# Kernel optimization log

Hardware: AMD Instinct MI355X
Metric: run time of the kernel (lower is better)

The kernel has to match this reference:

```python
import jax, jax.numpy as jnp
import numpy as np

DIM = 384
HEADS = 12
WS = 7
HID = 4 * 256  # FFN hidden is hard-coded default 1024, NOT 4*dim
EPS = 1e-5


def layernorm(x, g, b):
    mu = jnp.mean(x, axis=-1, keepdims=True)
    var = jnp.mean(jnp.square(x - mu), axis=-1, keepdims=True)
    return (x - mu) * jax.lax.rsqrt(var + EPS) * g + b


def setup_inputs() -> dict:
    key = jax.random.key(0)
    ks = jax.random.split(key, 12)
    s = 0.02
    return {
        "x": jax.random.normal(ks[0], (32, DIM, 56, 56), dtype=jnp.float32),
        "ln1_g": jnp.ones((DIM,), jnp.float32),
        "ln1_b": jnp.zeros((DIM,), jnp.float32),
        "qkv_w": jax.random.normal(ks[1], (3 * DIM, DIM), jnp.float32) * s,
        "qkv_b": jnp.zeros((3 * DIM,), jnp.float32),
        "proj_w": jax.random.normal(ks[2], (DIM, DIM), jnp.float32) * s,
        "proj_b": jnp.zeros((DIM,), jnp.float32),
        "ln2_g": jnp.ones((DIM,), jnp.float32),
        "ln2_b": jnp.zeros((DIM,), jnp.float32),
        "fc1_w": jax.random.normal(ks[3], (HID, DIM), jnp.float32) * s,
        "fc1_b": jnp.zeros((HID,), jnp.float32),
        "fc2_w": jax.random.normal(ks[4], (DIM, HID), jnp.float32) * s,
        "fc2_b": jnp.zeros((DIM,), jnp.float32),
    }


def window_attention(x, qkv_w, qkv_b, proj_w, proj_b):
    # x: [B, H, W, C] channels-last
    B, H, W, C = x.shape
    Wh, Ww = H // WS, W // WS
    # partition: [B*Wh*Ww, WS*WS, C]
    w = x.reshape(B, Wh, WS, Ww, WS, C).transpose(0, 1, 3, 2, 4, 5)
    w = w.reshape(B * Wh * Ww, WS * WS, C)
    Bn, N, _ = w.shape
    hd = C // HEADS
    qkv = w @ qkv_w.T + qkv_b  # [Bn, N, 3C]
    qkv = qkv.reshape(Bn, N, 3, HEADS, hd).transpose(2, 0, 3, 1, 4)
    q, k, v = qkv[0], qkv[1], qkv[2]  # each [Bn, h, N, hd]
    attn = jnp.einsum('bhnd,bhmd->bhnm', q, k) * (hd ** -0.5)
    attn = jax.nn.softmax(attn, axis=-1)
    o = jnp.einsum('bhnm,bhmd->bhnd', attn, v)
    o = o.transpose(0, 2, 1, 3).reshape(Bn, N, C)
    o = o @ proj_w.T + proj_b
    # reverse
    o = o.reshape(B, Wh, Ww, WS, WS, C).transpose(0, 1, 3, 2, 4, 5)
    return o.reshape(B, H, W, C)


def reference(x, ln1_g, ln1_b, qkv_w, qkv_b, proj_w, proj_b,
              ln2_g, ln2_b, fc1_w, fc1_b, fc2_w, fc2_b):
    # x: [B, C, H, W]
    residual = x
    h = x.transpose(0, 2, 3, 1)  # [B,H,W,C]
    h = layernorm(h, ln1_g, ln1_b)
    h = window_attention(h, qkv_w, qkv_b, proj_w, proj_b)
    x = h.transpose(0, 3, 1, 2) + residual
    residual = x
    h = x.transpose(0, 2, 3, 1)
    h = layernorm(h, ln2_g, ln2_b)
    h = jax.nn.gelu(h @ fc1_w.T + fc1_b, approximate=False)
    h = h @ fc2_w.T + fc2_b
    return h.transpose(0, 3, 1, 2) + residual
```

## Files before the change

kernel.cpp:

```cpp
#include <hip/hip_runtime.h>
#include <cstdint>
#include <cmath>

#define DIM 384
#define HEADS 12
#define TOKENS 100352
#define HW_ 3136
#define NWIN 2048

typedef __attribute__((ext_vector_type(8))) short short8;
typedef __attribute__((ext_vector_type(4))) short short4v;
typedef __attribute__((ext_vector_type(2))) short short2v;
typedef __attribute__((ext_vector_type(4))) float f32x4;

#define AS1 __attribute__((address_space(1)))
#define AS3 __attribute__((address_space(3)))

__device__ __forceinline__ short f2b(float f){
  unsigned u = __builtin_bit_cast(unsigned, f);
  u += 0x7FFFu + ((u >> 16) & 1u);
  return (short)(u >> 16);
}
__device__ __forceinline__ float b2f(short h){
  unsigned u = ((unsigned)(unsigned short)h) << 16;
  return __builtin_bit_cast(float, u);
}

__device__ __forceinline__ void gload_lds16(const short* g, short* l){
  __builtin_amdgcn_global_load_lds((AS1 void*)(g), (AS3 void*)(l), 16, 0, 0);
}

__global__ void k_cvt(const float* __restrict__ s, short* __restrict__ d, int n){
  int i = blockIdx.x*256 + threadIdx.x;
  if (i < n) d[i] = f2b(s[i]);
}

__global__ __launch_bounds__(256) void k_ln1(const float* __restrict__ x,
    const float* __restrict__ gam, const float* __restrict__ bet,
    short* __restrict__ ln1, short* __restrict__ xr)
{
  __shared__ float red0[256];
  __shared__ float red1[256];
  __shared__ float mus[64], rss[64];
  __shared__ short lnc[64*36];
  __shared__ short xc[64*36];
  int t = threadIdx.x;
  int blk = blockIdx.x;
  int b = blk / 49;
  int hw0 = (blk % 49) * 64;
  int p = t & 63, cq = t >> 6;
  const float* xb = x + (long)b*DIM*HW_ + hw0 + p;
  float s = 0.f, sq = 0.f;
  for (int i = 0; i < 96; i++){
    int c = i*4 + cq;
    float v = xb[(long)c*HW_];
    s += v; sq += v*v;
  }
  red0[t] = s; red1[t] = sq;
  __syncthreads();
  if (t < 64){
    float ts = red0[t] + red0[t+64] + red0[t+128] + red0[t+192];
    float tq = red1[t] + red1[t+64] + red1[t+128] + red1[t+192];
    float mu = ts * (1.f/DIM);
    float var = tq * (1.f/DIM) - mu*mu;
    mus[t] = mu;
    rss[t] = rsqrtf(var + 1e-5f);
  }
  __syncthreads();
  float mu_p = mus[p], rs_p = rss[p];
  int p2 = t >> 2, q4 = t & 3;
  int hwp2 = hw0 + p2;
  int h2 = hwp2 / 56, w2 = hwp2 % 56;
  int wt2 = ((b*8 + h2/7)*8 + w2/7)*49 + (h2%7)*7 + (w2%7);
  long lnbase = (long)wt2*DIM;
  long xrbase = (long)(b*HW_ + hwp2)*DIM;
  for (int cc0 = 0; cc0 < DIM; cc0 += 32){
    #pragma unroll
    for (int u = 0; u < 8; u++){
      int c = cc0 + cq*8 + u;
      float v = xb[(long)c*HW_];
      float nv = (v - mu_p)*rs_p*gam[c] + bet[c];
      lnc[p*36 + cq*8 + u] = f2b(nv);
      xc[p*36 + cq*8 + u] = f2b(v);
    }
    __syncthreads();
    short8 av, bv;
    #pragma unroll
    for (int u = 0; u < 8; u++){
      av[u] = lnc[p2*36 + q4*8 + u];
      bv[u] = xc[p2*36 + q4*8 + u];
    }
    *(short8*)(ln1 + lnbase + cc0 + q4*8) = av;
    *(short8*)(xr + xrbase + cc0 + q4*8) = bv;
    __syncthreads();
  }
}

#define EPI_BIAS 0
#define EPI_PROJ 1
#define EPI_GELU 2
#define EPI_RES  3

template<int EPI>
__global__ __launch_bounds__(256) void k_gemm(
    const short* __restrict__ A, const short* __restrict__ B,
    const float* __restrict__ bias, short* __restrict__ out,
    const short* __restrict__ res, int M, int N, int K, int ntiles)
{
  __shared__ float smemf[8448];
  short* AsP = (short*)smemf;
  short* BsP = (short*)(smemf + 4096);
  float* E   = smemf;

  int nwg = gridDim.x;
  int orig = blockIdx.x;
  int bid = (orig & 7) * (nwg >> 3) + (orig >> 3);
  int nt = bid % ntiles, mt = bid / ntiles;
  int m0 = mt*128, n0 = nt*128;
  int t = threadIdx.x;
  int lane = t & 63, wv = t >> 6;
  int wm = wv >> 1, wn = wv & 1;
  int gg = lane >> 4, cc = lane & 15;

  int srow = t >> 2;
  int skc = ((t & 3) ^ (srow & 3)) << 3;
  const short* Ab = A + (long)(m0 + srow)*K + skc;
  const short* Bb = B + (long)(n0 + srow)*K + skc;
  long rowstep = 64L*K;

  int goff = (gg << 3) ^ ((cc & 3) << 3);

  f32x4 acc[4][4];
  #pragma unroll
  for (int i=0;i<4;i++)
    #pragma unroll
    for (int j=0;j<4;j++) acc[i][j] = (f32x4){0.f,0.f,0.f,0.f};

  gload_lds16(Ab,           AsP + t*8);
  gload_lds16(Ab + rowstep, AsP + (t+256)*8);
  gload_lds16(Bb,           BsP + t*8);
  gload_lds16(Bb + rowstep, BsP + (t+256)*8);

  int nk = K >> 5;
  for (int kt = 0; kt < nk; kt++){
    int cur = kt & 1;
    __syncthreads();
    if (kt + 1 < nk){
      int nxt = cur ^ 1;
      long ko = (long)(kt + 1) << 5;
      gload_lds16(Ab + ko,           AsP + nxt*4096 + t*8);
      gload_lds16(Ab + ko + rowstep, AsP + nxt*4096 + (t+256)*8);
      gload_lds16(Bb + ko,           BsP + nxt*4096 + t*8);
      gload_lds16(Bb + ko + rowstep, BsP + nxt*4096 + (t+256)*8);
    }
    const short* Ac = AsP + cur*4096;
    const short* Bc = BsP + cur*4096;
    short8 af[4], bfv[4];
    #pragma unroll
    for (int mi=0;mi<4;mi++) af[mi] = *(const short8*)(Ac + (wm*64 + mi*16 + cc)*32 + goff);
    #pragma unroll
    for (int ni=0;ni<4;ni++) bfv[ni] = *(const short8*)(Bc + (wn*64 + ni*16 + cc)*32 + goff);
    #pragma unroll
    for (int mi=0;mi<4;mi++)
      #pragma unroll
      for (int ni=0;ni<4;ni++)
        acc[mi][ni] = __builtin_amdgcn_mfma_f32_16x16x32_bf16(af[mi], bfv[ni], acc[mi][ni], 0, 0, 0);
  }

  #pragma unroll
  for (int p = 0; p < 2; p++){
    __syncthreads();
    #pragma unroll
    for (int mh = 0; mh < 2; mh++){
      #pragma unroll
      for (int r = 0; r < 4; r++){
        int crow = wm*32 + mh*16 + gg*4 + r;
        float* Er = E + crow*132 + wn*64 + cc;
        Er[0]  = acc[mh*2 + p][0][r];
        Er[16] = acc[mh*2 + p][1][r];
        Er[32] = acc[mh*2 + p][2][r];
        Er[48] = acc[mh*2 + p][3][r];
      }
    }
    __syncthreads();
    #pragma unroll
    for (int jj = 0; jj < 8; jj++){
      int unit = jj*256 + t;
      int crow = unit >> 5, chunk = unit & 31;
      int rr = crow & 15, mh = (crow >> 4) & 1, wmr = crow >> 5;
      int row = m0 + wmr*64 + (mh*2 + p)*16 + rr;
      int col = n0 + chunk*4;
      f32x4 v = *(const f32x4*)(E + crow*132 + chunk*4);
      f32x4 bv = *(const f32x4*)(bias + col);
      long orow;
      if constexpr (EPI == EPI_PROJ) {
        int b = row / HW_; int rem = row % HW_;
        int wid = rem / 49, idx = rem % 49;
        int hh = (wid >> 3)*7 + idx/7;
        int ww = (wid & 7)*7 + idx%7;
        orow = (long)(b*HW_ + hh*56 + ww)*N;
      } else {
        orow = (long)row*N;
      }
      float vv[4];
      #pragma unroll
      for (int j = 0; j < 4; j++){
        vv[j] = v[j] + bv[j];
        if constexpr (EPI == EPI_GELU)
          vv[j] = 0.5f*vv[j]*(1.f + erff(vv[j]*0.70710678118654752f));
      }
      if constexpr (EPI == EPI_PROJ || EPI == EPI_RES){
        short4v rv = *(const short4v*)(res + orow + col);
        #pragma unroll
        for (int j = 0; j < 4; j++) vv[j] += b2f(rv[j]);
      }
      short4v ov;
      #pragma unroll
      for (int j = 0; j < 4; j++) ov[j] = f2b(vv[j]);
      *(short4v*)(out + orow + col) = ov;
    }
  }
}

__global__ __launch_bounds__(256) void k_attn(const short* __restrict__ qkv, short* __restrict__ o)
{
  __shared__ short lds[4*7424];
  int t = threadIdx.x;
  int lane = t & 63, wv = t >> 6;
  int w = blockIdx.x;
  short* Qs = lds + wv*7424;
  short* Ks = Qs + 2560;
  short* Vt = Ks + 2560;
  short* Pl = Qs;
  int g = lane >> 4, c = lane & 15;
  int nrow = lane >> 2;
  int dc = (lane & 3) * 8;
  const float scale = 0.17677669529663687f;
  for (int hh = 0; hh < 3; hh++){
    int h = wv + hh*4;
    __syncthreads();
    long base = (long)w*49*1152 + h*32;
    #pragma unroll
    for (int it = 0; it < 4; it++){
      int n = it*16 + nrow;
      short8 vq = {0,0,0,0,0,0,0,0};
      short8 vk = vq, vvv = vq;
      if (n < 49){
        vq  = *(const short8*)(qkv + base + (long)n*1152 + dc);
        vk  = *(const short8*)(qkv + base + (long)n*1152 + 384 + dc);
        vvv = *(const short8*)(qkv + base + (long)n*1152 + 768 + dc);
      }
      *(short8*)(Qs + n*40 + dc) = vq;
      *(short8*)(Ks + n*40 + dc) = vk;
      #pragma unroll
      for (int u = 0; u < 8; u++) Vt[(dc+u)*72 + n] = vvv[u];
    }
    __syncthreads();
    f32x4 sacc[4][4];
    #pragma unroll
    for (int i=0;i<4;i++)
      #pragma unroll
      for (int j=0;j<4;j++) sacc[i][j] = (f32x4){0.f,0.f,0.f,0.f};
    short8 kf[4];
    #pragma unroll
    for (int ni=0;ni<4;ni++) kf[ni] = *(const short8*)(Ks + (ni*16 + c)*40 + g*8);
    #pragma unroll
    for (int mi=0;mi<4;mi++){
      short8 a = *(const short8*)(Qs + (mi*16 + c)*40 + g*8);
      #pragma unroll
      for (int ni=0;ni<4;ni++)
        sacc[mi][ni] = __builtin_amdgcn_mfma_f32_16x16x32_bf16(a, kf[ni], sacc[mi][ni], 0, 0, 0);
    }
    #pragma unroll
    for (int mi=0;mi<4;mi++){
      #pragma unroll
      for (int r=0;r<4;r++){
        float v0 = sacc[mi][0][r]*scale;
        float v1 = sacc[mi][1][r]*scale;
        float v2 = sacc[mi][2][r]*scale;
        float v3 = (c >= 1) ? -1e30f : sacc[mi][3][r]*scale;
        float mx = fmaxf(fmaxf(v0,v1), fmaxf(v2,v3));
        #pragma unroll
        for (int off=1; off<16; off<<=1) mx = fmaxf(mx, __shfl_xor(mx, off));
        float e0 = __expf(v0-mx), e1 = __expf(v1-mx), e2 = __expf(v2-mx), e3 = __expf(v3-mx);
        float sm = e0+e1+e2+e3;
        #pragma unroll
        for (int off=1; off<16; off<<=1) sm += __shfl_xor(sm, off);
        float inv = 1.f/sm;
        int prow = mi*16 + g*4 + r;
        Pl[prow*72 +      c] = f2b(e0*inv);
        Pl[prow*72 + 16 + c] = f2b(e1*inv);
        Pl[prow*72 + 32 + c] = f2b(e2*inv);
        Pl[prow*72 + 48 + c] = f2b(e3*inv);
      }
    }
    __syncthreads();
    f32x4 oacc[4][2];
    #pragma unroll
    for (int i=0;i<4;i++){ oacc[i][0] = (f32x4){0.f,0.f,0.f,0.f}; oacc[i][1] = oacc[i][0]; }
    #pragma unroll
    for (int ks=0; ks<2; ks++){
      short8 bb0 = *(const short8*)(Vt + (c)*72      + ks*32 + g*8);
      short8 bb1 = *(const short8*)(Vt + (16 + c)*72 + ks*32 + g*8);
      #pragma unroll
      for (int mi=0;mi<4;mi++){
        short8 aa = *(const short8*)(Pl + (mi*16 + c)*72 + ks*32 + g*8);
        oacc[mi][0] = __builtin_amdgcn_mfma_f32_16x16x32_bf16(aa, bb0, oacc[mi][0], 0, 0, 0);
        oacc[mi][1] = __builtin_amdgcn_mfma_f32_16x16x32_bf16(aa, bb1, oacc[mi][1], 0, 0, 0);
      }
    }
    #pragma unroll
    for (int mi=0;mi<4;mi++){
      #pragma unroll
      for (int r=0;r<4;r++){
        int row = mi*16 + g*4 + r;
        if (row < 49){
          long ob = ((long)w*49 + row)*384 + h*32;
          o[ob + c]      = f2b(oacc[mi][0][r]);
          o[ob + 16 + c] = f2b(oacc[mi][1][r]);
        }
      }
    }
  }
}

__global__ __launch_bounds__(256) void k_ln2(const short* __restrict__ x2,
  const float* __restrict__ gam, const float* __restrict__ bet, short* __restrict__ o)
{
  int t = threadIdx.x, lane = t & 63, wv = t >> 6;
  long row = (long)blockIdx.x*4 + wv;
  const short* xr = x2 + row*DIM;
  short4v a = *(const short4v*)(xr + lane*4);
  short2v b2 = *(const short2v*)(xr + 256 + lane*2);
  float f[6] = {b2f(a[0]),b2f(a[1]),b2f(a[2]),b2f(a[3]),b2f(b2[0]),b2f(b2[1])};
  float s = 0.f, sq = 0.f;
  #pragma unroll
  for (int i=0;i<6;i++){ s += f[i]; sq += f[i]*f[i]; }
  #pragma unroll
  for (int off=1; off<64; off<<=1){ s += __shfl_xor(s, off); sq += __shfl_xor(sq, off); }
  float mu = s*(1.f/DIM);
  float var = sq*(1.f/DIM) - mu*mu;
  float rs = rsqrtf(var + 1e-5f);
  int c0 = lane*4, c1 = 256 + lane*2;
  short4v oa; short2v ob;
  #pragma unroll
  for (int i=0;i<4;i++) oa[i] = f2b((f[i]-mu)*rs*gam[c0+i] + bet[c0+i]);
  #pragma unroll
  for (int j=0;j<2;j++) ob[j] = f2b((f[4+j]-mu)*rs*gam[c1+j] + bet[c1+j]);
  *(short4v*)(o + row*DIM + c0) = oa;
  *(short2v*)(o + row*DIM + c1) = ob;
}

__global__ __launch_bounds__(256) void k_out(const short* __restrict__ s, float* __restrict__ o)
{
  __shared__ short tile[64*392];
  int t = threadIdx.x;
  long tok0 = (long)blockIdx.x*64;
  int b = (int)(tok0 / HW_), hw0 = (int)(tok0 % HW_);
  #pragma unroll
  for (int i=0;i<12;i++){
    int unit = i*256 + t;
    int tok = unit / 48, slot = unit % 48;
    short8 v = *(const short8*)(s + (tok0+tok)*DIM + slot*8);
    int slotS = slot ^ (tok & 3);
    *(short8*)(tile + tok*392 + slotS*8) = v;
  }
  __syncthreads();
  int p = t & 63;
  int cq = t >> 6;
  for (int j=0;j<96;j++){
    int c = j*4 + cq;
    int sw = (c >> 3) ^ (p & 3);
    o[((long)b*DIM + c)*HW_ + hw0 + p] = b2f(tile[p*392 + sw*8 + (c & 7)]);
  }
}

extern "C" void kernel_launch(void* const* d_in, const int* in_sizes, int n_in,
                              void* d_out, int out_size, void* d_ws, size_t ws_size,
                              hipStream_t stream) {
  (void)in_sizes; (void)n_in; (void)out_size; (void)ws_size;
  const float* x      = (const float*)d_in[0];
  const float* ln1_g  = (const float*)d_in[1];
  const float* ln1_b  = (const float*)d_in[2];
  const float* qkv_w  = (const float*)d_in[3];
  const float* qkv_b  = (const float*)d_in[4];
  const float* proj_w = (const float*)d_in[5];
  const float* proj_b = (const float*)d_in[6];
  const float* ln2_g  = (const float*)d_in[7];
  const float* ln2_b  = (const float*)d_in[8];
  const float* fc1_w  = (const float*)d_in[9];
  const float* fc1_b  = (const float*)d_in[10];
  const float* fc2_w  = (const float*)d_in[11];
  const float* fc2_b  = (const float*)d_in[12];

  char* ws = (char*)d_ws;
  short* buf1 = (short*)(ws);
  short* buf2 = (short*)(ws + 231211008L);
  short* buf3 = (short*)(ws + 308281344L);
  short* buf4 = (short*)(ws + 385351680L);
  short* buf5 = (short*)(ws + 462422016L);
  short* wq = (short*)(ws + 539492352L);
  short* wp = wq + 442368;
  short* w1 = wp + 147456;
  short* w2 = w1 + 393216;

  k_cvt<<<dim3((442368+255)/256), dim3(256), 0, stream>>>(qkv_w, wq, 442368);
  k_cvt<<<dim3((147456+255)/256), dim3(256), 0, stream>>>(proj_w, wp, 147456);
  k_cvt<<<dim3((393216+255)/256), dim3(256), 0, stream>>>(fc1_w, w1, 393216);
  k_cvt<<<dim3((393216+255)/256), dim3(256), 0, stream>>>(fc2_w, w2, 393216);

  k_ln1<<<dim3(1568), dim3(256), 0, stream>>>(x, ln1_g, ln1_b, buf2, buf5);

  k_gemm<EPI_BIAS><<<dim3(784*9), dim3(256), 0, stream>>>(buf2, wq, qkv_b, buf1, nullptr,
                                                          TOKENS, 1152, 384, 9);
  k_attn<<<dim3(NWIN), dim3(256), 0, stream>>>(buf1, buf3);

  k_gemm<EPI_PROJ><<<dim3(784*3), dim3(256), 0, stream>>>(buf3, wp, proj_b, buf4, buf5,
                                                          TOKENS, 384, 384, 3);
  k_ln2<<<dim3(TOKENS/4), dim3(256), 0, stream>>>(buf4, ln2_g, ln2_b, buf2);

  k_gemm<EPI_GELU><<<dim3(784*8), dim3(256), 0, stream>>>(buf2, w1, fc1_b, buf1, nullptr,
                                                          TOKENS, 1024, 384, 8);
  k_gemm<EPI_RES><<<dim3(784*3), dim3(256), 0, stream>>>(buf1, w2, fc2_b, buf3, buf4,
                                                         TOKENS, 384, 1024, 3);
  k_out<<<dim3(1568), dim3(256), 0, stream>>>(buf3, (float*)d_out);
}
```

Before: 795.8 us.

## Enlarge GEMM tiles to 256x128 with three-stage LDS pipeline

Each GEMM workgroup now computes a 256x128 output tile instead of 128x128, which halves the grid sizes and raises reuse of the B operand. LDS is now split into three buffers, loads run two stages ahead, and explicit vmcnt waits replace the per-step syncthreads. The XOR swizzle on LDS tile addresses is removed, and launch bounds now ask for two waves per SIMD. The change trades higher register and LDS use, and possible LDS bank conflicts from the unswizzled layout, for fewer global loads and more overlap of memory latency.

```diff
diff --git a/kernel.cpp b/kernel.cpp
--- a/kernel.cpp
+++ b/kernel.cpp
@@ -101,85 +101,85 @@
 #define EPI_GELU 2
 #define EPI_RES  3
 
+__device__ __forceinline__ void stage_tile(const short* __restrict__ A,
+    const short* __restrict__ B, int K, int m0, int n0, int kk,
+    short* buf, int t)
+{
+  int rowA = t >> 2, slot = (t & 3) << 3;
+  const short* As = A + (long)(m0 + rowA)*K + kk + slot;
+  gload_lds16(As,                buf + t*8);
+  gload_lds16(As + 64L*K,        buf + (t+256)*8);
+  gload_lds16(As + 128L*K,       buf + (t+512)*8);
+  gload_lds16(As + 192L*K,       buf + (t+768)*8);
+  const short* Bs = B + (long)(n0 + rowA)*K + kk + slot;
+  gload_lds16(Bs,                buf + 8192 + t*8);
+  gload_lds16(Bs + 64L*K,        buf + 8192 + (t+256)*8);
+}
+
 template<int EPI>
-__global__ __launch_bounds__(256) void k_gemm(
+__global__ __launch_bounds__(256, 2) void k_gemm(
     const short* __restrict__ A, const short* __restrict__ B,
     const float* __restrict__ bias, short* __restrict__ out,
     const short* __restrict__ res, int M, int N, int K, int ntiles)
 {
-  __shared__ float smemf[8448];
-  short* AsP = (short*)smemf;
-  short* BsP = (short*)(smemf + 4096);
-  float* E   = smemf;
+  __shared__ short sbuf[36864];
+  float* E = (float*)sbuf;
 
   int nwg = gridDim.x;
   int orig = blockIdx.x;
   int bid = (orig & 7) * (nwg >> 3) + (orig >> 3);
   int nt = bid % ntiles, mt = bid / ntiles;
-  int m0 = mt*128, n0 = nt*128;
+  int m0 = mt*256, n0 = nt*128;
   int t = threadIdx.x;
   int lane = t & 63, wv = t >> 6;
   int wm = wv >> 1, wn = wv & 1;
   int gg = lane >> 4, cc = lane & 15;
 
-  int srow = t >> 2;
-  int skc = ((t & 3) ^ (srow & 3)) << 3;
-  const short* Ab = A + (long)(m0 + srow)*K + skc;
-  const short* Bb = B + (long)(n0 + srow)*K + skc;
-  long rowstep = 64L*K;
-
-  int goff = (gg << 3) ^ ((cc & 3) << 3);
-
-  f32x4 acc[4][4];
-  #pragma unroll
-  for (int i=0;i<4;i++)
+  f32x4 acc[8][4];
+  #pragma unroll
+  for (int i=0;i<8;i++)
     #pragma unroll
     for (int j=0;j<4;j++) acc[i][j] = (f32x4){0.f,0.f,0.f,0.f};
 
-  gload_lds16(Ab,           AsP + t*8);
-  gload_lds16(Ab + rowstep, AsP + (t+256)*8);
-  gload_lds16(Bb,           BsP + t*8);
-  gload_lds16(Bb + rowstep, BsP + (t+256)*8);
-
   int nk = K >> 5;
+  stage_tile(A, B, K, m0, n0, 0,  sbuf,         t);
+  stage_tile(A, B, K, m0, n0, 32, sbuf + 12288, t);
+
   for (int kt = 0; kt < nk; kt++){
-    int cur = kt & 1;
-    __syncthreads();
-    if (kt + 1 < nk){
-      int nxt = cur ^ 1;
-      long ko = (long)(kt + 1) << 5;
-      gload_lds16(Ab + ko,           AsP + nxt*4096 + t*8);
-      gload_lds16(Ab + ko + rowstep, AsP + nxt*4096 + (t+256)*8);
-      gload_lds16(Bb + ko,           BsP + nxt*4096 + t*8);
-      gload_lds16(Bb + ko + rowstep, BsP + nxt*4096 + (t+256)*8);
-    }
-    const short* Ac = AsP + cur*4096;
-    const short* Bc = BsP + cur*4096;
-    short8 af[4], bfv[4];
-    #pragma unroll
-    for (int mi=0;mi<4;mi++) af[mi] = *(const short8*)(Ac + (wm*64 + mi*16 + cc)*32 + goff);
-    #pragma unroll
-    for (int ni=0;ni<4;ni++) bfv[ni] = *(const short8*)(Bc + (wn*64 + ni*16 + cc)*32 + goff);
-    #pragma unroll
-    for (int mi=0;mi<4;mi++)
+    if (kt + 1 < nk) { asm volatile("s_waitcnt vmcnt(6)" ::: "memory"); }
+    else             { asm volatile("s_waitcnt vmcnt(0)" ::: "memory"); }
+    __builtin_amdgcn_s_barrier();
+    if (kt + 2 < nk){
+      int nb = kt + 2; nb -= (nb >= 3) ? ((nb/3)*3) : 0;
+      stage_tile(A, B, K, m0, n0, (kt+2) << 5, sbuf + ((kt+2)%3)*12288, t);
+      (void)nb;
+    }
+    const short* Ac = sbuf + (kt%3)*12288;
+    const short* Bc = Ac + 8192;
+    short8 af[8], bf[4];
+    #pragma unroll
+    for (int mi=0;mi<8;mi++) af[mi] = *(const short8*)(Ac + (wm*128 + mi*16 + cc)*32 + gg*8);
+    #pragma unroll
+    for (int ni=0;ni<4;ni++) bf[ni] = *(const short8*)(Bc + (wn*64 + ni*16 + cc)*32 + gg*8);
+    #pragma unroll
+    for (int mi=0;mi<8;mi++)
       #pragma unroll
       for (int ni=0;ni<4;ni++)
-        acc[mi][ni] = __builtin_amdgcn_mfma_f32_16x16x32_bf16(af[mi], bfv[ni], acc[mi][ni], 0, 0, 0);
-  }
-
-  #pragma unroll
-  for (int p = 0; p < 2; p++){
-    __syncthreads();
-    #pragma unroll
-    for (int mh = 0; mh < 2; mh++){
+        acc[mi][ni] = __builtin_amdgcn_mfma_f32_16x16x32_bf16(af[mi], bf[ni], acc[mi][ni], 0, 0, 0);
+  }
+
+  #pragma unroll
+  for (int p = 0; p < 4; p++){
+    __syncthreads();
+    #pragma unroll
+    for (int u = 0; u < 2; u++){
       #pragma unroll
       for (int r = 0; r < 4; r++){
-        int crow = wm*32 + mh*16 + gg*4 + r;
-        float* Er = E + crow*132 + wn*64 + cc;
-        Er[0]  = acc[mh*2 + p][0][r];
-        Er[16] = acc[mh*2 + p][1][r];
-        Er[32] = acc[mh*2 + p][2][r];
-        Er[48] = acc[mh*2 + p][3][r];
+        float* Er = E + (wm*32 + u*16 + gg*4 + r)*132 + wn*64 + cc;
+        Er[0]  = acc[2*p + u][0][r];
+        Er[16] = acc[2*p + u][1][r];
+        Er[32] = acc[2*p + u][2][r];
+        Er[48] = acc[2*p + u][3][r];
       }
     }
     __syncthreads();
@@ -187,8 +187,8 @@
     for (int jj = 0; jj < 8; jj++){
       int unit = jj*256 + t;
       int crow = unit >> 5, chunk = unit & 31;
-      int rr = crow & 15, mh = (crow >> 4) & 1, wmr = crow >> 5;
-      int row = m0 + wmr*64 + (mh*2 + p)*16 + rr;
+      int rr = crow & 15, uu = (crow >> 4) & 1, wmr = crow >> 5;
+      int row = m0 + wmr*128 + (2*p + uu)*16 + rr;
       int col = n0 + chunk*4;
       f32x4 v = *(const f32x4*)(E + crow*132 + chunk*4);
       f32x4 bv = *(const f32x4*)(bias + col);
@@ -411,17 +411,17 @@
 
   k_ln1<<<dim3(1568), dim3(256), 0, stream>>>(x, ln1_g, ln1_b, buf2, buf5);
 
-  k_gemm<EPI_BIAS><<<dim3(784*9), dim3(256), 0, stream>>>(buf2, wq, qkv_b, buf1, nullptr,
+  k_gemm<EPI_BIAS><<<dim3(392*9), dim3(256), 0, stream>>>(buf2, wq, qkv_b, buf1, nullptr,
                                                           TOKENS, 1152, 384, 9);
   k_attn<<<dim3(NWIN), dim3(256), 0, stream>>>(buf1, buf3);
 
-  k_gemm<EPI_PROJ><<<dim3(784*3), dim3(256), 0, stream>>>(buf3, wp, proj_b, buf4, buf5,
+  k_gemm<EPI_PROJ><<<dim3(392*3), dim3(256), 0, stream>>>(buf3, wp, proj_b, buf4, buf5,
                                                           TOKENS, 384, 384, 3);
   k_ln2<<<dim3(TOKENS/4), dim3(256), 0, stream>>>(buf4, ln2_g, ln2_b, buf2);
 
-  k_gemm<EPI_GELU><<<dim3(784*8), dim3(256), 0, stream>>>(buf2, w1, fc1_b, buf1, nullptr,
+  k_gemm<EPI_GELU><<<dim3(392*8), dim3(256), 0, stream>>>(buf2, w1, fc1_b, buf1, nullptr,
                                                           TOKENS, 1024, 384, 8);
-  k_gemm<EPI_RES><<<dim3(784*3), dim3(256), 0, stream>>>(buf1, w2, fc2_b, buf3, buf4,
+  k_gemm<EPI_RES><<<dim3(392*3), dim3(256), 0, stream>>>(buf1, w2, fc2_b, buf3, buf4,
                                                          TOKENS, 384, 1024, 3);
   k_out<<<dim3(1568), dim3(256), 0, stream>>>(buf3, (float*)d_out);
 }
```

Measured after the change: 833.3 us. +4.7%, slower.

## Triple-buffer GEMM LDS pipeline with explicit vmcnt waits and compile-time K

Applied to the files above, without the earlier changes.

Replaces the double-buffered K loop in the bf16 GEMM with a three-stage LDS ring that prefetches two K-tiles ahead. It uses explicit s_waitcnt vmcnt(4) plus a raw barrier in place of __syncthreads, so one tile's loads stay in flight during compute. K becomes a template parameter so the loop fully unrolls, and launch bounds request 3 waves per SIMD. LDS use grows to 48KB per block, which may limit occupancy, and the hand-written waitcnt assumes the exact count of outstanding loads.

```diff
diff --git a/kernel.cpp b/kernel.cpp
--- a/kernel.cpp
+++ b/kernel.cpp
@@ -101,16 +101,14 @@
 #define EPI_GELU 2
 #define EPI_RES  3
 
-template<int EPI>
-__global__ __launch_bounds__(256) void k_gemm(
+template<int EPI, int K>
+__global__ __launch_bounds__(256, 3) void k_gemm(
     const short* __restrict__ A, const short* __restrict__ B,
     const float* __restrict__ bias, short* __restrict__ out,
-    const short* __restrict__ res, int M, int N, int K, int ntiles)
+    const short* __restrict__ res, int M, int N, int ntiles)
 {
-  __shared__ float smemf[8448];
-  short* AsP = (short*)smemf;
-  short* BsP = (short*)(smemf + 4096);
-  float* E   = smemf;
+  __shared__ short sbuf[24576];
+  float* E = (float*)sbuf;
 
   int nwg = gridDim.x;
   int orig = blockIdx.x;
@@ -123,10 +121,9 @@
   int gg = lane >> 4, cc = lane & 15;
 
   int srow = t >> 2;
-  int skc = ((t & 3) ^ (srow & 3)) << 3;
+  int skc  = ((t & 3) ^ (srow & 3)) << 3;
   const short* Ab = A + (long)(m0 + srow)*K + skc;
   const short* Bb = B + (long)(n0 + srow)*K + skc;
-  long rowstep = 64L*K;
 
   int goff = (gg << 3) ^ ((cc & 3) << 3);
 
@@ -136,35 +133,42 @@
     #pragma unroll
     for (int j=0;j<4;j++) acc[i][j] = (f32x4){0.f,0.f,0.f,0.f};
 
-  gload_lds16(Ab,           AsP + t*8);
-  gload_lds16(Ab + rowstep, AsP + (t+256)*8);
-  gload_lds16(Bb,           BsP + t*8);
-  gload_lds16(Bb + rowstep, BsP + (t+256)*8);
-
-  int nk = K >> 5;
-  for (int kt = 0; kt < nk; kt++){
-    int cur = kt & 1;
-    __syncthreads();
-    if (kt + 1 < nk){
-      int nxt = cur ^ 1;
-      long ko = (long)(kt + 1) << 5;
-      gload_lds16(Ab + ko,           AsP + nxt*4096 + t*8);
-      gload_lds16(Ab + ko + rowstep, AsP + nxt*4096 + (t+256)*8);
-      gload_lds16(Bb + ko,           BsP + nxt*4096 + t*8);
-      gload_lds16(Bb + ko + rowstep, BsP + nxt*4096 + (t+256)*8);
-    }
-    const short* Ac = AsP + cur*4096;
-    const short* Bc = BsP + cur*4096;
-    short8 af[4], bfv[4];
+  constexpr int NK = K >> 5;
+
+  #pragma unroll
+  for (int pt = 0; pt < 2; pt++){
+    short* sb = sbuf + pt*8192;
+    gload_lds16(Ab + pt*32,           sb + t*8);
+    gload_lds16(Ab + pt*32 + 64*K,    sb + (t+256)*8);
+    gload_lds16(Bb + pt*32,           sb + 4096 + t*8);
+    gload_lds16(Bb + pt*32 + 64*K,    sb + 4096 + (t+256)*8);
+  }
+
+  #pragma unroll
+  for (int kt = 0; kt < NK; kt++){
+    if (kt + 1 < NK) { asm volatile("s_waitcnt vmcnt(4) lgkmcnt(0)" ::: "memory"); }
+    else             { asm volatile("s_waitcnt vmcnt(0) lgkmcnt(0)" ::: "memory"); }
+    __builtin_amdgcn_s_barrier();
+    if (kt + 2 < NK){
+      short* sb = sbuf + ((kt+2)%3)*8192;
+      const int kk = (kt+2)*32;
+      gload_lds16(Ab + kk,          sb + t*8);
+      gload_lds16(Ab + kk + 64*K,   sb + (t+256)*8);
+      gload_lds16(Bb + kk,          sb + 4096 + t*8);
+      gload_lds16(Bb + kk + 64*K,   sb + 4096 + (t+256)*8);
+    }
+    const short* Ac = sbuf + (kt%3)*8192;
+    const short* Bc = Ac + 4096;
+    short8 af[4], bf[4];
     #pragma unroll
     for (int mi=0;mi<4;mi++) af[mi] = *(const short8*)(Ac + (wm*64 + mi*16 + cc)*32 + goff);
     #pragma unroll
-    for (int ni=0;ni<4;ni++) bfv[ni] = *(const short8*)(Bc + (wn*64 + ni*16 + cc)*32 + goff);
+    for (int ni=0;ni<4;ni++) bf[ni] = *(const short8*)(Bc + (wn*64 + ni*16 + cc)*32 + goff);
     #pragma unroll
     for (int mi=0;mi<4;mi++)
       #pragma unroll
       for (int ni=0;ni<4;ni++)
-        acc[mi][ni] = __builtin_amdgcn_mfma_f32_16x16x32_bf16(af[mi], bfv[ni], acc[mi][ni], 0, 0, 0);
+        acc[mi][ni] = __builtin_amdgcn_mfma_f32_16x16x32_bf16(af[mi], bf[ni], acc[mi][ni], 0, 0, 0);
   }
 
   #pragma unroll
@@ -411,17 +415,17 @@
 
   k_ln1<<<dim3(1568), dim3(256), 0, stream>>>(x, ln1_g, ln1_b, buf2, buf5);
 
-  k_gemm<EPI_BIAS><<<dim3(784*9), dim3(256), 0, stream>>>(buf2, wq, qkv_b, buf1, nullptr,
-                                                          TOKENS, 1152, 384, 9);
+  k_gemm<EPI_BIAS,384><<<dim3(784*9), dim3(256), 0, stream>>>(buf2, wq, qkv_b, buf1, nullptr,
+                                                              TOKENS, 1152, 9);
   k_attn<<<dim3(NWIN), dim3(256), 0, stream>>>(buf1, buf3);
 
-  k_gemm<EPI_PROJ><<<dim3(784*3), dim3(256), 0, stream>>>(buf3, wp, proj_b, buf4, buf5,
-                                                          TOKENS, 384, 384, 3);
+  k_gemm<EPI_PROJ,384><<<dim3(784*3), dim3(256), 0, stream>>>(buf3, wp, proj_b, buf4, buf5,
+                                                              TOKENS, 384, 3);
   k_ln2<<<dim3(TOKENS/4), dim3(256), 0, stream>>>(buf4, ln2_g, ln2_b, buf2);
 
-  k_gemm<EPI_GELU><<<dim3(784*8), dim3(256), 0, stream>>>(buf2, w1, fc1_b, buf1, nullptr,
-                                                          TOKENS, 1024, 384, 8);
-  k_gemm<EPI_RES><<<dim3(784*3), dim3(256), 0, stream>>>(buf1, w2, fc2_b, buf3, buf4,
-                                                         TOKENS, 384, 1024, 3);
+  k_gemm<EPI_GELU,384><<<dim3(784*8), dim3(256), 0, stream>>>(buf2, w1, fc1_b, buf1, nullptr,
+                                                              TOKENS, 1024, 8);
+  k_gemm<EPI_RES,1024><<<dim3(784*3), dim3(256), 0, stream>>>(buf1, w2, fc2_b, buf3, buf4,
+                                                              TOKENS, 384, 3);
   k_out<<<dim3(1568), dim3(256), 0, stream>>>(buf3, (float*)d_out);
 }
```

Result: slower. 859.0 us (+7.9%).

## Fuse proj GEMM with LayerNorm2 and fc2 GEMM with NCHW output transpose

Applied to the files above, without the earlier changes.

Replaces the proj GEMM plus separate LN2 kernel with a single kernel that computes a full 384-column row tile, adds the residual, writes x2 and then computes LayerNorm in the epilogue. The fc2 GEMM epilogue now adds the residual and writes fp32 output directly in NCHW layout, which removes the k_out transpose kernel. K is made a template parameter so the k-loop can be fully unrolled. Together these remove two kernel launches and their intermediate buffer round trips. The cost is a heavier projln kernel with larger LDS use, and strided transposed global stores in the final epilogue.

```diff
diff --git a/kernel.cpp b/kernel.cpp
--- a/kernel.cpp
+++ b/kernel.cpp
@@ -97,17 +97,17 @@
 }
 
 #define EPI_BIAS 0
-#define EPI_PROJ 1
 #define EPI_GELU 2
 #define EPI_RES  3
-
-template<int EPI>
+#define EPI_OUT  4
+
+template<int EPI, int K>
 __global__ __launch_bounds__(256) void k_gemm(
     const short* __restrict__ A, const short* __restrict__ B,
     const float* __restrict__ bias, short* __restrict__ out,
-    const short* __restrict__ res, int M, int N, int K, int ntiles)
+    const short* __restrict__ res, int M, int N, int ntiles)
 {
-  __shared__ float smemf[8448];
+  __shared__ float smemf[8512];
   short* AsP = (short*)smemf;
   short* BsP = (short*)(smemf + 4096);
   float* E   = smemf;
@@ -126,7 +126,7 @@
   int skc = ((t & 3) ^ (srow & 3)) << 3;
   const short* Ab = A + (long)(m0 + srow)*K + skc;
   const short* Bb = B + (long)(n0 + srow)*K + skc;
-  long rowstep = 64L*K;
+  const long rowstep = 64L*K;
 
   int goff = (gg << 3) ^ ((cc & 3) << 3);
 
@@ -135,19 +135,21 @@
   for (int i=0;i<4;i++)
     #pragma unroll
     for (int j=0;j<4;j++) acc[i][j] = (f32x4){0.f,0.f,0.f,0.f};
+
+  constexpr int NK = K >> 5;
 
   gload_lds16(Ab,           AsP + t*8);
   gload_lds16(Ab + rowstep, AsP + (t+256)*8);
   gload_lds16(Bb,           BsP + t*8);
   gload_lds16(Bb + rowstep, BsP + (t+256)*8);
 
-  int nk = K >> 5;
-  for (int kt = 0; kt < nk; kt++){
-    int cur = kt & 1;
-    __syncthreads();
-    if (kt + 1 < nk){
-      int nxt = cur ^ 1;
-      long ko = (long)(kt + 1) << 5;
+  #pragma unroll
+  for (int kt = 0; kt < NK; kt++){
+    const int cur = kt & 1;
+    __syncthreads();
+    if (kt + 1 < NK){
+      const int nxt = cur ^ 1;
+      const long ko = (long)(kt + 1) << 5;
       gload_lds16(Ab + ko,           AsP + nxt*4096 + t*8);
       gload_lds16(Ab + ko + rowstep, AsP + nxt*4096 + (t+256)*8);
       gload_lds16(Bb + ko,           BsP + nxt*4096 + t*8);
@@ -167,58 +169,214 @@
         acc[mi][ni] = __builtin_amdgcn_mfma_f32_16x16x32_bf16(af[mi], bfv[ni], acc[mi][ni], 0, 0, 0);
   }
 
-  #pragma unroll
-  for (int p = 0; p < 2; p++){
-    __syncthreads();
-    #pragma unroll
-    for (int mh = 0; mh < 2; mh++){
-      #pragma unroll
-      for (int r = 0; r < 4; r++){
-        int crow = wm*32 + mh*16 + gg*4 + r;
-        float* Er = E + crow*132 + wn*64 + cc;
-        Er[0]  = acc[mh*2 + p][0][r];
-        Er[16] = acc[mh*2 + p][1][r];
-        Er[32] = acc[mh*2 + p][2][r];
-        Er[48] = acc[mh*2 + p][3][r];
-      }
-    }
-    __syncthreads();
-    #pragma unroll
-    for (int jj = 0; jj < 8; jj++){
-      int unit = jj*256 + t;
-      int crow = unit >> 5, chunk = unit & 31;
-      int rr = crow & 15, mh = (crow >> 4) & 1, wmr = crow >> 5;
-      int row = m0 + wmr*64 + (mh*2 + p)*16 + rr;
-      int col = n0 + chunk*4;
-      f32x4 v = *(const f32x4*)(E + crow*132 + chunk*4);
-      f32x4 bv = *(const f32x4*)(bias + col);
-      long orow;
-      if constexpr (EPI == EPI_PROJ) {
-        int b = row / HW_; int rem = row % HW_;
-        int wid = rem / 49, idx = rem % 49;
-        int hh = (wid >> 3)*7 + idx/7;
-        int ww = (wid & 7)*7 + idx%7;
-        orow = (long)(b*HW_ + hh*56 + ww)*N;
-      } else {
-        orow = (long)row*N;
-      }
-      float vv[4];
-      #pragma unroll
-      for (int j = 0; j < 4; j++){
-        vv[j] = v[j] + bv[j];
-        if constexpr (EPI == EPI_GELU)
-          vv[j] = 0.5f*vv[j]*(1.f + erff(vv[j]*0.70710678118654752f));
-      }
-      if constexpr (EPI == EPI_PROJ || EPI == EPI_RES){
-        short4v rv = *(const short4v*)(res + orow + col);
-        #pragma unroll
-        for (int j = 0; j < 4; j++) vv[j] += b2f(rv[j]);
-      }
-      short4v ov;
-      #pragma unroll
-      for (int j = 0; j < 4; j++) ov[j] = f2b(vv[j]);
-      *(short4v*)(out + orow + col) = ov;
-    }
+  if constexpr (EPI == EPI_OUT) {
+    float* outf = (float*)out;
+    #pragma unroll
+    for (int p = 0; p < 2; p++){
+      __syncthreads();
+      if (wm == p){
+        #pragma unroll
+        for (int mi=0;mi<4;mi++){
+          #pragma unroll
+          for (int r=0;r<4;r++){
+            float* Er = E + (mi*16 + gg*4 + r)*133 + wn*64 + cc;
+            Er[0]  = acc[mi][0][r];
+            Er[16] = acc[mi][1][r];
+            Er[32] = acc[mi][2][r];
+            Er[48] = acc[mi][3][r];
+          }
+        }
+      }
+      __syncthreads();
+      #pragma unroll
+      for (int jj = 0; jj < 8; jj++){
+        int unit = jj*256 + t;
+        int crow = unit >> 5, chunk = unit & 31;
+        int row = m0 + p*64 + crow;
+        f32x4 v = *(const f32x4*)(E + crow*133 + chunk*4);
+        f32x4 bv = *(const f32x4*)(bias + n0 + chunk*4);
+        short4v rv = *(const short4v*)(res + (long)row*N + n0 + chunk*4);
+        #pragma unroll
+        for (int j = 0; j < 4; j++) v[j] += bv[j] + b2f(rv[j]);
+        *(f32x4*)(E + crow*133 + chunk*4) = v;
+      }
+      __syncthreads();
+      #pragma unroll
+      for (int jj = 0; jj < 32; jj++){
+        int unit = jj*256 + t;
+        int c = unit >> 6, rl = unit & 63;
+        int token = m0 + p*64 + rl;
+        int b = token / HW_;
+        int hw = token - b*HW_;
+        outf[((long)b*DIM + n0 + c)*HW_ + hw] = E[rl*133 + c];
+      }
+    }
+  } else {
+    #pragma unroll
+    for (int p = 0; p < 2; p++){
+      __syncthreads();
+      #pragma unroll
+      for (int mh = 0; mh < 2; mh++){
+        #pragma unroll
+        for (int r = 0; r < 4; r++){
+          int crow = wm*32 + mh*16 + gg*4 + r;
+          float* Er = E + crow*133 + wn*64 + cc;
+          Er[0]  = acc[mh*2 + p][0][r];
+          Er[16] = acc[mh*2 + p][1][r];
+          Er[32] = acc[mh*2 + p][2][r];
+          Er[48] = acc[mh*2 + p][3][r];
+        }
+      }
+      __syncthreads();
+      #pragma unroll
+      for (int jj = 0; jj < 8; jj++){
+        int unit = jj*256 + t;
+        int crow = unit >> 5, chunk = unit & 31;
+        int rr = crow & 15, mh = (crow >> 4) & 1, wmr = crow >> 5;
+        int row = m0 + wmr*64 + (mh*2 + p)*16 + rr;
+        int col = n0 + chunk*4;
+        f32x4 v = *(const f32x4*)(E + crow*133 + chunk*4);
+        f32x4 bv = *(const f32x4*)(bias + col);
+        long orow = (long)row*N;
+        float vv[4];
+        #pragma unroll
+        for (int j = 0; j < 4; j++){
+          vv[j] = v[j] + bv[j];
+          if constexpr (EPI == EPI_GELU)
+            vv[j] = 0.5f*vv[j]*(1.f + erff(vv[j]*0.70710678118654752f));
+        }
+        if constexpr (EPI == EPI_RES){
+          short4v rv = *(const short4v*)(res + orow + col);
+          #pragma unroll
+          for (int j = 0; j < 4; j++) vv[j] += b2f(rv[j]);
+        }
+        short4v ov;
+        #pragma unroll
+        for (int j = 0; j < 4; j++) ov[j] = f2b(vv[j]);
+        *(short4v*)(out + orow + col) = ov;
+      }
+    }
+  }
+}
+
+template<int K>
+__global__ __launch_bounds__(256, 2) void k_projln(
+    const short* __restrict__ A, const short* __restrict__ B,
+    const float* __restrict__ bias, const short* __restrict__ res,
+    const float* __restrict__ gam, const float* __restrict__ bet,
+    short* __restrict__ x2, short* __restrict__ ln)
+{
+  __shared__ short sb[28672];
+  short* X = sb;
+
+  int nwg = gridDim.x;
+  int orig = blockIdx.x;
+  int bid = (orig & 7) * (nwg >> 3) + (orig >> 3);
+  int m0 = bid*64;
+  int t = threadIdx.x;
+  int lane = t & 63, wv = t >> 6;
+  int gg = lane >> 4, cc = lane & 15;
+
+  int srow = t >> 2;
+  int skc = ((t & 3) ^ (srow & 3)) << 3;
+  const short* Abp = A + (long)(m0 + srow)*K + skc;
+  const short* Bbp = B + (long)srow*K + skc;
+
+  int goff = (gg << 3) ^ ((cc & 3) << 3);
+
+  f32x4 acc[4][6];
+  #pragma unroll
+  for (int i=0;i<4;i++)
+    #pragma unroll
+    for (int j=0;j<6;j++) acc[i][j] = (f32x4){0.f,0.f,0.f,0.f};
+
+  constexpr int NK = K >> 5;
+
+  gload_lds16(Abp, sb + t*8);
+  #pragma unroll
+  for (int j = 0; j < 6; j++)
+    gload_lds16(Bbp + (long)j*64*K, sb + 4096 + j*2048 + t*8);
+
+  #pragma unroll
+  for (int kt = 0; kt < NK; kt++){
+    const int cur = kt & 1;
+    __syncthreads();
+    if (kt + 1 < NK){
+      const int nxt = cur ^ 1;
+      const long ko = (long)(kt + 1) << 5;
+      gload_lds16(Abp + ko, sb + nxt*2048 + t*8);
+      #pragma unroll
+      for (int j = 0; j < 6; j++)
+        gload_lds16(Bbp + ko + (long)j*64*K, sb + 4096 + nxt*12288 + j*2048 + t*8);
+    }
+    const short* Ac = sb + cur*2048;
+    const short* Bc = sb + 4096 + cur*12288;
+    short8 af[4], bfv[6];
+    #pragma unroll
+    for (int mi=0;mi<4;mi++) af[mi] = *(const short8*)(Ac + (mi*16 + cc)*32 + goff);
+    #pragma unroll
+    for (int ni=0;ni<6;ni++) bfv[ni] = *(const short8*)(Bc + (wv*96 + ni*16 + cc)*32 + goff);
+    #pragma unroll
+    for (int mi=0;mi<4;mi++)
+      #pragma unroll
+      for (int ni=0;ni<6;ni++)
+        acc[mi][ni] = __builtin_amdgcn_mfma_f32_16x16x32_bf16(af[mi], bfv[ni], acc[mi][ni], 0, 0, 0);
+  }
+
+  __syncthreads();
+  #pragma unroll
+  for (int mi=0;mi<4;mi++){
+    #pragma unroll
+    for (int ni=0;ni<6;ni++){
+      int col = wv*96 + ni*16 + cc;
+      float bcol = bias[col];
+      #pragma unroll
+      for (int r=0;r<4;r++){
+        X[(mi*16 + gg*4 + r)*392 + col] = f2b(acc[mi][ni][r] + bcol);
+      }
+    }
+  }
+  __syncthreads();
+  int row = t >> 2, q = t & 3;
+  int rw = m0 + row;
+  int b = rw / HW_; int rem = rw % HW_;
+  int wid = rem / 49, idx = rem % 49;
+  int hh = (wid >> 3)*7 + idx/7;
+  int ww = (wid & 7)*7 + idx%7;
+  long r_out = (long)b*HW_ + hh*56 + ww;
+  int c0 = q*96;
+
+  short8 o8[12];
+  float s = 0.f, sq = 0.f;
+  #pragma unroll
+  for (int i = 0; i < 12; i++){
+    short8 xv = *(const short8*)(X + row*392 + c0 + i*8);
+    short8 rv = *(const short8*)(res + r_out*DIM + c0 + i*8);
+    #pragma unroll
+    for (int u = 0; u < 8; u++){
+      float v = b2f(xv[u]) + b2f(rv[u]);
+      short h = f2b(v);
+      o8[i][u] = h;
+      float vb = b2f(h);
+      s += vb; sq += vb*vb;
+    }
+    *(short8*)(x2 + r_out*DIM + c0 + i*8) = o8[i];
+  }
+  s  += __shfl_xor(s, 1);  s  += __shfl_xor(s, 2);
+  sq += __shfl_xor(sq, 1); sq += __shfl_xor(sq, 2);
+  float mu = s * (1.f/DIM);
+  float var = sq * (1.f/DIM) - mu*mu;
+  float rs = rsqrtf(var + 1e-5f);
+  #pragma unroll
+  for (int i = 0; i < 12; i++){
+    short8 l8;
+    #pragma unroll
+    for (int u = 0; u < 8; u++){
+      int c = c0 + i*8 + u;
+      float f = b2f(o8[i][u]);
+      l8[u] = f2b((f - mu)*rs*gam[c] + bet[c]);
+    }
+    *(short8*)(ln + r_out*DIM + c0 + i*8) = l8;
   }
 }
 
@@ -321,57 +479,6 @@
         }
       }
     }
-  }
-}
-
-__global__ __launch_bounds__(256) void k_ln2(const short* __restrict__ x2,
-  const float* __restrict__ gam, const float* __restrict__ bet, short* __restrict__ o)
-{
-  int t = threadIdx.x, lane = t & 63, wv = t >> 6;
-  long row = (long)blockIdx.x*4 + wv;
-  const short* xr = x2 + row*DIM;
-  short4v a = *(const short4v*)(xr + lane*4);
-  short2v b2 = *(const short2v*)(xr + 256 + lane*2);
-  float f[6] = {b2f(a[0]),b2f(a[1]),b2f(a[2]),b2f(a[3]),b2f(b2[0]),b2f(b2[1])};
-  float s = 0.f, sq = 0.f;
-  #pragma unroll
-  for (int i=0;i<6;i++){ s += f[i]; sq += f[i]*f[i]; }
-  #pragma unroll
-  for (int off=1; off<64; off<<=1){ s += __shfl_xor(s, off); sq += __shfl_xor(sq, off); }
-  float mu = s*(1.f/DIM);
-  float var = sq*(1.f/DIM) - mu*mu;
-  float rs = rsqrtf(var + 1e-5f);
-  int c0 = lane*4, c1 = 256 + lane*2;
-  short4v oa; short2v ob;
-  #pragma unroll
-  for (int i=0;i<4;i++) oa[i] = f2b((f[i]-mu)*rs*gam[c0+i] + bet[c0+i]);
-  #pragma unroll
-  for (int j=0;j<2;j++) ob[j] = f2b((f[4+j]-mu)*rs*gam[c1+j] + bet[c1+j]);
-  *(short4v*)(o + row*DIM + c0) = oa;
-  *(short2v*)(o + row*DIM + c1) = ob;
-}
-
-__global__ __launch_bounds__(256) void k_out(const short* __restrict__ s, float* __restrict__ o)
-{
-  __shared__ short tile[64*392];
-  int t = threadIdx.x;
-  long tok0 = (long)blockIdx.x*64;
-  int b = (int)(tok0 / HW_), hw0 = (int)(tok0 % HW_);
-  #pragma unroll
-  for (int i=0;i<12;i++){
-    int unit = i*256 + t;
-    int tok = unit / 48, slot = unit % 48;
-    short8 v = *(const short8*)(s + (tok0+tok)*DIM + slot*8);
-    int slotS = slot ^ (tok & 3);
-    *(short8*)(tile + tok*392 + slotS*8) = v;
-  }
-  __syncthreads();
-  int p = t & 63;
-  int cq = t >> 6;
-  for (int j=0;j<96;j++){
-    int c = j*4 + cq;
-    int sw = (c >> 3) ^ (p & 3);
-    o[((long)b*DIM + c)*HW_ + hw0 + p] = b2f(tile[p*392 + sw*8 + (c & 7)]);
   }
 }
 
@@ -411,17 +518,15 @@
 
   k_ln1<<<dim3(1568), dim3(256), 0, stream>>>(x, ln1_g, ln1_b, buf2, buf5);
 
-  k_gemm<EPI_BIAS><<<dim3(784*9), dim3(256), 0, stream>>>(buf2, wq, qkv_b, buf1, nullptr,
-                                                          TOKENS, 1152, 384, 9);
+  k_gemm<EPI_BIAS,384><<<dim3(784*9), dim3(256), 0, stream>>>(buf2, wq, qkv_b, buf1, nullptr,
+                                                              TOKENS, 1152, 9);
   k_attn<<<dim3(NWIN), dim3(256), 0, stream>>>(buf1, buf3);
 
-  k_gemm<EPI_PROJ><<<dim3(784*3), dim3(256), 0, stream>>>(buf3, wp, proj_b, buf4, buf5,
-                                                          TOKENS, 384, 384, 3);
-  k_ln2<<<dim3(TOKENS/4), dim3(256), 0, stream>>>(buf4, ln2_g, ln2_b, buf2);
-
-  k_gemm<EPI_GELU><<<dim3(784*8), dim3(256), 0, stream>>>(buf2, w1, fc1_b, buf1, nullptr,
-                                                          TOKENS, 1024, 384, 8);
-  k_gemm<EPI_RES><<<dim3(784*3), dim3(256), 0, stream>>>(buf1, w2, fc2_b, buf3, buf4,
-                                                         TOKENS, 384, 1024, 3);
-  k_out<<<dim3(1568), dim3(256), 0, stream>>>(buf3, (float*)d_out);
-}
+  k_projln<384><<<dim3(1568), dim3(256), 0, stream>>>(buf3, wp, proj_b, buf5,
+                                                      ln2_g, ln2_b, buf4, buf2);
+
+  k_gemm<EPI_GELU,384><<<dim3(784*8), dim3(256), 0, stream>>>(buf2, w1, fc1_b, buf1, nullptr,
+                                                              TOKENS, 1024, 8);
+  k_gemm<EPI_OUT,1024><<<dim3(784*3), dim3(256), 0, stream>>>(buf1, w2, fc2_b, (short*)d_out, buf4,
+                                                              TOKENS, 384, 3);
+}
```

Result: slower. 879.6 us (+10.5%).
